# Performance work log

Hardware: AMD Instinct MI355X
Metric: run time of the kernel (lower is better)

Reference implementation:

```python
import jax, jax.numpy as jnp
import numpy as np

D_MODEL = 2048
NUM_HEADS = 16
MAX_SEQ_LEN = 2048
ROPE_BASE = 10000.0


def _rope(x, start_pos):
    # x: [B, S, D]; rotates interleaved pairs then concatenates halves,
    # exactly matching the torch module (NOT the usual interleaved output).
    B, S, D = x.shape
    theta = 1.0 / (ROPE_BASE ** (jnp.arange(0, D, 2, dtype=jnp.float32) / D))  # [D/2]
    pos = jnp.arange(start_pos, start_pos + S, dtype=jnp.float32)[:, None]      # [S,1]
    ang = pos * theta[None, :]                                                  # [S, D/2]
    cos, sin = jnp.cos(ang), jnp.sin(ang)
    x1 = x[..., 0::2]
    x2 = x[..., 1::2]
    return jnp.concatenate([x1 * cos - x2 * sin, x1 * sin + x2 * cos], axis=-1)


def setup_inputs() -> dict:
    key = jax.random.key(0)
    kx, kq, kk, kv, ko = jax.random.split(key, 5)
    B, S, D = 4, 2048, D_MODEL
    scale = 1.0 / np.sqrt(D)
    return {
        "x": jax.random.normal(kx, (B, S, D), dtype=jnp.float32),
        "w_q": jax.random.normal(kq, (D, D), dtype=jnp.float32) * scale,
        "w_k": jax.random.normal(kk, (D, D), dtype=jnp.float32) * scale,
        "w_v": jax.random.normal(kv, (D, D), dtype=jnp.float32) * scale,
        "w_o": jax.random.normal(ko, (D, D), dtype=jnp.float32) * scale,
        "start_pos": 0,
    }


def reference(x, w_q, w_k, w_v, w_o, start_pos):
    B, S, D = x.shape
    H = NUM_HEADS
    hd = D // H
    # Linear(d, d, bias=False): y = x @ W^T
    Q = _rope(x @ w_q.T, start_pos)
    K = _rope(x @ w_k.T, start_pos)
    V = x @ w_v.T
    q = Q.reshape(B, S, H, hd).transpose(0, 2, 1, 3)  # [B,H,S,hd]
    k = K.reshape(B, S, H, hd).transpose(0, 2, 1, 3)
    v = V.reshape(B, S, H, hd).transpose(0, 2, 1, 3)
    # cache=None path: kv_len == S
    attn = jnp.einsum("bhqd,bhkd->bhqk", q, k) / jnp.sqrt(jnp.float32(hd))
    # causal mask: key j attends only if j <= i + (kv_len - seq_len); here offset=0
    kv_len = k.shape[2]
    offset = kv_len - S
    i = jnp.arange(S)[:, None]
    j = jnp.arange(kv_len)[None, :]
    attn = jnp.where(j > i + offset, jnp.float32(-jnp.inf), attn)
    attn = jax.nn.softmax(attn, axis=-1)
    # dropout: inference mode (identity)
    out = jnp.einsum("bhqk,bhkd->bhqd", attn, v)
    out = out.transpose(0, 2, 1, 3).reshape(B, S, D)
    output = out @ w_o.T
    return (output, k, v)
```

## Files before the change

### kernel.cpp

```cpp
#include <hip/hip_runtime.h>
#include <hip/hip_bf16.h>

typedef __attribute__((ext_vector_type(4))) float f32x4;
typedef __attribute__((ext_vector_type(8))) short s16x8;

#define SEQ 2048
#define DM  2048
#define NH  16
#define HD  128

__device__ __forceinline__ unsigned short f2b(float f){
  unsigned int u = __builtin_bit_cast(unsigned int, f);
  u += 0x7fffu + ((u >> 16) & 1u);
  return (unsigned short)(u >> 16);
}
__device__ __forceinline__ float b2f(unsigned short h){
  unsigned int u = ((unsigned int)h) << 16;
  return __builtin_bit_cast(float, u);
}
__device__ __forceinline__ f32x4 mfma16(s16x8 a, s16x8 b, f32x4 c){
  return __builtin_amdgcn_mfma_f32_16x16x32_bf16(a, b, c, 0, 0, 0);
}

__global__ __launch_bounds__(256)
void convert_kernel(const float* __restrict__ x,  const float* __restrict__ wq,
                    const float* __restrict__ wk, const float* __restrict__ wv,
                    const float* __restrict__ wo,
                    unsigned short* __restrict__ xb,
                    unsigned short* __restrict__ wfused,
                    unsigned short* __restrict__ wob)
{
  size_t e = ((size_t)blockIdx.x * 256 + threadIdx.x) * 8;
  const float* src; unsigned short* dst;
  if (e < 16777216){ src = x + e; dst = xb + e; }
  else if (e < 29360128){
    size_t o = e - 16777216;
    int sel = (int)(o >> 22);
    const float* w = sel == 0 ? wq : (sel == 1 ? wk : wv);
    src = w + (o & 4194303); dst = wfused + o;
  } else {
    size_t o = e - 29360128;
    src = wo + o; dst = wob + o;
  }
  float4 a = ((const float4*)src)[0];
  float4 b = ((const float4*)src)[1];
  s16x8 v;
  v[0]=(short)f2b(a.x); v[1]=(short)f2b(a.y); v[2]=(short)f2b(a.z); v[3]=(short)f2b(a.w);
  v[4]=(short)f2b(b.x); v[5]=(short)f2b(b.y); v[6]=(short)f2b(b.z); v[7]=(short)f2b(b.w);
  *(s16x8*)dst = v;
}

template<int MODE>
__global__ __launch_bounds__(512, 2)
void gemm8(const unsigned short* __restrict__ A,
           const unsigned short* __restrict__ B,
           unsigned short* __restrict__ qr, unsigned short* __restrict__ kr,
           float* __restrict__ koutf,
           float* __restrict__ voutf, unsigned short* __restrict__ vt,
           float* __restrict__ outf, const int* __restrict__ sp)
{
  extern __shared__ char lds[];
  const int tid  = threadIdx.x;
  const int lane = tid & 63;
  const int w    = tid >> 6;
  const int wr   = w >> 2;
  const int wc   = w & 3;
  const int l15  = lane & 15;
  const int lhi  = lane >> 4;
  const int rq   = lhi << 2;

  int bid = blockIdx.x;
  int x8 = bid & 7, j = bid >> 3;
  int mb, nb;
  if (MODE == 0){ nb = 3*x8 + (j % 3); mb = j / 3; }
  else          { nb = x8;             mb = j; }
  const int m0 = mb * 256, n0 = nb * 256;

  const int sp0 = (MODE == 0) ? sp[0] : 0;

  const unsigned short* Abase = A + (size_t)m0 * 2048;
  const unsigned short* Bbase = B + (size_t)n0 * 2048;

  f32x4 accL[4][4] = {};
  f32x4 accH[4][4] = {};
  s16x8 af[4], bf[4];

  auto STAGE = [&](const unsigned short* gbase, int ldsoff, int t, int ks){
    #pragma unroll
    for (int r2 = 0; r2 < 2; r2++){
      int p  = r2*8192 + w*1024 + (lane << 4);
      int lo = p ^ (((p >> 7) & 3) << 4);
      int row = lo >> 6, colB = lo & 63;
      __builtin_amdgcn_global_load_lds(
        (const __attribute__((address_space(1))) void*)
          (gbase + (size_t)row*2048 + t*64 + ks*32 + (colB >> 1)),
        (__attribute__((address_space(3))) void*)(lds + ldsoff + r2*8192 + w*1024),
        16, 0, 0);
    }
  };
  auto SA = [&](int t, int ks){ STAGE(Abase, (t&1)*65536 +         ks*16384, t, ks); };
  auto SB = [&](int t, int ks){ STAGE(Bbase, (t&1)*65536 + 32768 + ks*16384, t, ks); };

  auto LDA4 = [&](int slot, int ks, int i0){
    const char* base = lds + slot*65536 + ks*16384;
    #pragma unroll
    for (int i = 0; i < 4; i++){
      int row = wr*128 + (i0 + i)*16 + l15;
      int off = row*64 + lhi*16;
      af[i] = *(const s16x8*)(base + (off ^ (((row >> 1) & 3) << 4)));
    }
  };
  auto LDB4 = [&](int slot, int ks){
    const char* base = lds + slot*65536 + 32768 + ks*16384;
    #pragma unroll
    for (int j2 = 0; j2 < 4; j2++){
      int row = wc*64 + j2*16 + l15;
      int off = row*64 + lhi*16;
      bf[j2] = *(const s16x8*)(base + (off ^ (((row >> 1) & 3) << 4)));
    }
  };
  auto MM = [&](f32x4 (&ac)[4][4]){
    __builtin_amdgcn_s_setprio(1);
    #pragma unroll
    for (int i = 0; i < 4; i++)
      #pragma unroll
      for (int j2 = 0; j2 < 4; j2++)
        ac[i][j2] = mfma16(af[i], bf[j2], ac[i][j2]);
    __builtin_amdgcn_s_setprio(0);
  };

  SA(0,0); SB(0,0); SA(0,1); SB(0,1);
  asm volatile("s_waitcnt vmcnt(4)" ::: "memory");
  __builtin_amdgcn_s_barrier();

  #pragma unroll 2
  for (int t = 0; t < 31; t++){
    const int cs = t & 1;
    LDB4(cs, 0); LDA4(cs, 0, 0);
    SA(t+1, 0);
    __builtin_amdgcn_s_barrier();
    MM(accL);
    __builtin_amdgcn_s_barrier();
    LDA4(cs, 0, 4);
    SB(t+1, 0);
    __builtin_amdgcn_s_barrier();
    MM(accH);
    asm volatile("s_waitcnt vmcnt(4)" ::: "memory");
    __builtin_amdgcn_s_barrier();
    LDB4(cs, 1); LDA4(cs, 1, 0);
    SA(t+1, 1);
    __builtin_amdgcn_s_barrier();
    MM(accL);
    __builtin_amdgcn_s_barrier();
    LDA4(cs, 1, 4);
    SB(t+1, 1);
    __builtin_amdgcn_s_barrier();
    MM(accH);
    asm volatile("s_waitcnt vmcnt(4)" ::: "memory");
    __builtin_amdgcn_s_barrier();
  }
  {
    LDB4(1, 0); LDA4(1, 0, 0);
    __builtin_amdgcn_s_barrier();
    MM(accL);
    __builtin_amdgcn_s_barrier();
    LDA4(1, 0, 4);
    __builtin_amdgcn_s_barrier();
    MM(accH);
    asm volatile("s_waitcnt vmcnt(0)" ::: "memory");
    __builtin_amdgcn_s_barrier();
    LDB4(1, 1); LDA4(1, 1, 0);
    __builtin_amdgcn_s_barrier();
    MM(accL);
    __builtin_amdgcn_s_barrier();
    LDA4(1, 1, 4);
    __builtin_amdgcn_s_barrier();
    MM(accH);
  }

  if (MODE == 1){
    #pragma unroll
    for (int h2 = 0; h2 < 2; h2++){
      f32x4 (&ac)[4][4] = h2 ? accH : accL;
      int ibase = h2 * 4;
      #pragma unroll
      for (int i = 0; i < 4; i++)
        #pragma unroll
        for (int r = 0; r < 4; r++){
          int m = m0 + wr*128 + (ibase+i)*16 + rq + r;
          #pragma unroll
          for (int j2 = 0; j2 < 4; j2++)
            outf[(size_t)m*DM + n0 + wc*64 + j2*16 + l15] = ac[i][j2][r];
        }
    }
    return;
  }

  const int b  = m0 >> 11;
  const int s0 = m0 & 2047;

  if (nb < 16){
    const bool isK = (nb >= 8);
    unsigned short* dqk = isK ? kr : qr;
    const int fbase = (nb & 7) * 128;
    const int odd = lane & 1;

    __syncthreads();
    float2* T2 = (float2*)lds;
    float2* T1 = (float2*)(lds + 32768);
    for (int idx = tid; idx < 5120; idx += 512){
      int fl = idx & 127;
      float th = exp2f(-(float)(fbase + fl) * (13.287712379549449f / 1024.0f));
      float sn, cn;
      if (idx < 4096){
        __sincosf((float)(idx >> 7) * th, &sn, &cn);
        T2[idx] = make_float2(cn, sn);
      } else {
        int sh = (idx - 4096) >> 7;
        __sincosf((float)(sp0 + s0 + sh*32) * th, &sn, &cn);
        T1[idx - 4096] = make_float2(cn, sn);
      }
    }
    __syncthreads();

    #pragma unroll
    for (int h2 = 0; h2 < 2; h2++){
      f32x4 (&ac)[4][4] = h2 ? accH : accL;
      int ibase = h2 * 4;
      #pragma unroll
      for (int i = 0; i < 4; i++){
        #pragma unroll
        for (int r = 0; r < 4; r++){
          int srow = wr*128 + (ibase+i)*16 + rq + r;
          int s  = s0 + srow;
          int sh = srow >> 5, sl = srow & 31;
          #pragma unroll
          for (int j2 = 0; j2 < 4; j2++){
            float v  = ac[i][j2][r];
            float vx = __shfl_xor(v, 1);
            int nn_loc = wc*64 + j2*16 + l15;
            int fl = nn_loc >> 1;
            float2 a1 = T1[sh*128 + fl];
            float2 a2 = T2[sl*128 + fl];
            float cn = a1.x*a2.x - a1.y*a2.y;
            float sn = a1.y*a2.x + a1.x*a2.y;
            float x1 = odd ? vx : v;
            float x2 = odd ? v  : vx;
            float ov = odd ? (x1*sn + x2*cn) : (x1*cn - x2*sn);
            int c = fbase + fl + (odd ? 1024 : 0);
            size_t adr = ((size_t)(b*NH + (c >> 7))*SEQ + s)*HD + (c & 127);
            dqk[adr] = f2b(ov);
            if (isK) koutf[adr] = ov;
          }
        }
      }
    }
  } else {
    #pragma unroll
    for (int h2 = 0; h2 < 2; h2++){
      f32x4 (&ac)[4][4] = h2 ? accH : accL;
      int ibase = h2 * 4;
      #pragma unroll
      for (int i = 0; i < 4; i++){
        int sb = s0 + wr*128 + (ibase+i)*16 + rq;
        #pragma unroll
        for (int j2 = 0; j2 < 4; j2++){
          int d = (nb - 16)*256 + wc*64 + j2*16 + l15;
          int h = d >> 7, dd = d & 127;
          size_t vb = ((size_t)(b*NH + h)*SEQ + sb)*HD + dd;
          #pragma unroll
          for (int r = 0; r < 4; r++)
            voutf[vb + (size_t)r*HD] = ac[i][j2][r];
          ushort4 pk;
          pk.x = f2b(ac[i][j2][0]); pk.y = f2b(ac[i][j2][1]);
          pk.z = f2b(ac[i][j2][2]); pk.w = f2b(ac[i][j2][3]);
          *(ushort4*)(vt + ((size_t)(b*NH + h)*HD + dd)*SEQ + sb) = pk;
        }
      }
    }
  }
}

__global__ __launch_bounds__(256)
void attn_kernel(const unsigned short* __restrict__ qr,
                 const unsigned short* __restrict__ kr,
                 const unsigned short* __restrict__ vt,
                 unsigned short* __restrict__ attnout)
{
  const int pair = blockIdx.x;
  const int bh   = blockIdx.y;
  const int tid  = threadIdx.x;
  const int lane = tid & 63;
  const int w    = tid >> 6;

  __shared__ __align__(16) char Klds[64 * 256];
  __shared__ __align__(16) char Vlds[128 * 144];
  __shared__ __align__(16) char Plds[4][16 * 144];

  const int l15 = lane & 15;
  const int lhi = lane >> 4;
  const int rq  = lhi << 2;
  char* pw = &Plds[w][0];

  s16x8 ones;
  #pragma unroll
  for (int i = 0; i < 8; i++) ones[i] = (short)0x3F80;

  const int b = bh >> 4, h = bh & 15;

  for (int ph = 0; ph < 2; ph++){
    const int qtile = ph ? (31 - pair) : pair;
    const int q0w = qtile*64 + w*16;

    s16x8 qf[4];
    const unsigned short* qbase = qr + ((size_t)bh*SEQ + q0w + l15) * HD + lhi*8;
    #pragma unroll
    for (int c = 0; c < 4; c++) qf[c] = *(const s16x8*)(qbase + c*32);

    f32x4 o[8] = {};
    f32x4 osum = {};
    float mrow[4] = {-1e30f,-1e30f,-1e30f,-1e30f};

    const int ntiles = qtile + 1;
    for (int t = 0; t < ntiles; t++){
      const int kv0 = t * 64;
      __syncthreads();
      {
        int r = tid >> 2, q4 = tid & 3;
        const unsigned short* src = kr + ((size_t)bh*SEQ + kv0 + r) * HD + q4*32;
        int sw = (r & 15) << 4;
        char* drow = Klds + r*256;
        #pragma unroll
        for (int k = 0; k < 4; k++)
          *(s16x8*)(drow + ((q4*64 + k*16) ^ sw)) = *(const s16x8*)(src + k*8);
      }
      {
        int r = tid >> 1, h2 = tid & 1;
        const unsigned short* src = vt + ((size_t)bh*HD + r) * SEQ + kv0 + h2*32;
        char* drow = Vlds + r*144 + h2*64;
        #pragma unroll
        for (int k = 0; k < 4; k++)
          *(s16x8*)(drow + k*16) = *(const s16x8*)(src + k*8);
      }
      __syncthreads();

      f32x4 st[4];
      #pragma unroll
      for (int j = 0; j < 4; j++) st[j] = (f32x4){0.f,0.f,0.f,0.f};
      #pragma unroll
      for (int j = 0; j < 4; j++){
        int krw = j*16 + l15;
        int sw  = (krw & 15) << 4;
        #pragma unroll
        for (int c = 0; c < 4; c++){
          s16x8 kf = *(const s16x8*)(Klds + krw*256 + ((c*64 + lhi*16) ^ sw));
          st[j] = mfma16(qf[c], kf, st[j]);
        }
      }

      const float sc = 0.08838834764831845f;
      #pragma unroll
      for (int j = 0; j < 4; j++)
        #pragma unroll
        for (int r = 0; r < 4; r++){
          int qrow = q0w + rq + r;
          int kvc  = kv0 + j*16 + l15;
          st[j][r] = (kvc > qrow) ? -1e30f : st[j][r] * sc;
        }

      float mt[4];
      #pragma unroll
      for (int r = 0; r < 4; r++)
        mt[r] = fmaxf(fmaxf(st[0][r], st[1][r]), fmaxf(st[2][r], st[3][r]));
      #pragma unroll
      for (int mk = 1; mk < 16; mk <<= 1)
        #pragma unroll
        for (int r = 0; r < 4; r++) mt[r] = fmaxf(mt[r], __shfl_xor(mt[r], mk));

      int ok = 1;
      #pragma unroll
      for (int r = 0; r < 4; r++) ok &= (mt[r] <= mrow[r] + 8.0f) ? 1 : 0;
      if (!__all(ok)){
        float al[4];
        #pragma unroll
        for (int r = 0; r < 4; r++){
          float mn = fmaxf(mrow[r], mt[r]);
          al[r] = __expf(mrow[r] - mn);
          mrow[r] = mn;
        }
        #pragma unroll
        for (int c = 0; c < 8; c++)
          #pragma unroll
          for (int r = 0; r < 4; r++) o[c][r] *= al[r];
        #pragma unroll
        for (int r = 0; r < 4; r++) osum[r] *= al[r];
      }

      #pragma unroll
      for (int r = 0; r < 4; r++){
        char* prb = pw + (rq + r)*144;
        #pragma unroll
        for (int j = 0; j < 4; j++){
          float p = __expf(st[j][r] - mrow[r]);
          *(unsigned short*)(prb + (j*16 + l15)*2) = f2b(p);
        }
      }

      asm volatile("s_waitcnt lgkmcnt(0)" ::: "memory");

      #pragma unroll
      for (int ks = 0; ks < 2; ks++){
        s16x8 pa = *(const s16x8*)(pw + l15*144 + ks*64 + lhi*16);
        #pragma unroll
        for (int c = 0; c < 8; c++){
          int d = c*16 + l15;
          s16x8 vf = *(const s16x8*)(Vlds + d*144 + ks*64 + lhi*16);
          o[c] = mfma16(pa, vf, o[c]);
        }
        osum = mfma16(pa, ones, osum);
      }
    }

    #pragma unroll
    for (int r = 0; r < 4; r++){
      float inv = 1.0f / osum[r];
      int s2 = q0w + rq + r;
      size_t base = ((size_t)(b*SEQ + s2)) * DM + h*HD;
      #pragma unroll
      for (int c = 0; c < 8; c++)
        attnout[base + c*16 + l15] = f2b(o[c][r] * inv);
    }
  }
}

extern "C" void kernel_launch(void* const* d_in, const int* in_sizes, int n_in,
                              void* d_out, int out_size, void* d_ws, size_t ws_size,
                              hipStream_t stream)
{
  const float* x  = (const float*)d_in[0];
  const float* wq = (const float*)d_in[1];
  const float* wk = (const float*)d_in[2];
  const float* wv = (const float*)d_in[3];
  const float* wo = (const float*)d_in[4];
  const int*   sp = (const int*)d_in[5];

  float* out  = (float*)d_out;
  float* kout = out + 16777216;
  float* vout = out + 33554432;

  char* ws = (char*)d_ws;
  unsigned short* xb      = (unsigned short*)ws;
  unsigned short* wfused  = (unsigned short*)(ws + 33554432);
  unsigned short* wob     = (unsigned short*)(ws + 58720256);
  unsigned short* qr      = (unsigned short*)(ws + 67108864);
  unsigned short* kr      = (unsigned short*)(ws + 100663296);
  unsigned short* vt      = (unsigned short*)(ws + 134217728);
  unsigned short* attnout = (unsigned short*)ws;

  hipFuncSetAttribute((const void*)gemm8<0>,
                      hipFuncAttributeMaxDynamicSharedMemorySize, 131072);
  hipFuncSetAttribute((const void*)gemm8<1>,
                      hipFuncAttributeMaxDynamicSharedMemorySize, 131072);

  convert_kernel<<<16384, 256, 0, stream>>>(x, wq, wk, wv, wo, xb, wfused, wob);
  gemm8<0><<<768, 512, 131072, stream>>>(xb, wfused, qr, kr, kout,
                                         vout, vt, nullptr, sp);
  attn_kernel<<<dim3(16, 64), 256, 0, stream>>>(qr, kr, vt, attnout);
  gemm8<1><<<256, 512, 131072, stream>>>(attnout, wob, nullptr, nullptr,
                                         nullptr, nullptr, nullptr, out, nullptr);
}
```

Baseline: 599.9 us.

## Restructure GEMM main loop into 4-stage LDS ring with one barrier per tile

```diff
diff --git a/kernel.cpp b/kernel.cpp
--- a/kernel.cpp
+++ b/kernel.cpp
@@ -51,7 +51,7 @@
 }
 
 template<int MODE>
-__global__ __launch_bounds__(512, 2)
+__global__ __launch_bounds__(512, 1)
 void gemm8(const unsigned short* __restrict__ A,
            const unsigned short* __restrict__ B,
            unsigned short* __restrict__ qr, unsigned short* __restrict__ kr,
@@ -83,9 +83,8 @@
 
   f32x4 accL[4][4] = {};
   f32x4 accH[4][4] = {};
-  s16x8 af[4], bf[4];
-
-  auto STAGE = [&](const unsigned short* gbase, int ldsoff, int t, int ks){
+
+  auto STAGE = [&](const unsigned short* gbase, int slotoff, int t){
     #pragma unroll
     for (int r2 = 0; r2 < 2; r2++){
       int p  = r2*8192 + w*1024 + (lane << 4);
@@ -93,90 +92,67 @@
       int row = lo >> 6, colB = lo & 63;
       __builtin_amdgcn_global_load_lds(
         (const __attribute__((address_space(1))) void*)
-          (gbase + (size_t)row*2048 + t*64 + ks*32 + (colB >> 1)),
-        (__attribute__((address_space(3))) void*)(lds + ldsoff + r2*8192 + w*1024),
+          (gbase + (size_t)row*2048 + t*32 + (colB >> 1)),
+        (__attribute__((address_space(3))) void*)(lds + slotoff + r2*8192 + w*1024),
         16, 0, 0);
     }
   };
-  auto SA = [&](int t, int ks){ STAGE(Abase, (t&1)*65536 +         ks*16384, t, ks); };
-  auto SB = [&](int t, int ks){ STAGE(Bbase, (t&1)*65536 + 32768 + ks*16384, t, ks); };
-
-  auto LDA4 = [&](int slot, int ks, int i0){
-    const char* base = lds + slot*65536 + ks*16384;
+  auto LDA = [&](const char* base, int i0, s16x8* dst){
     #pragma unroll
     for (int i = 0; i < 4; i++){
       int row = wr*128 + (i0 + i)*16 + l15;
       int off = row*64 + lhi*16;
-      af[i] = *(const s16x8*)(base + (off ^ (((row >> 1) & 3) << 4)));
+      dst[i] = *(const s16x8*)(base + (off ^ (((row >> 1) & 3) << 4)));
     }
   };
-  auto LDB4 = [&](int slot, int ks){
-    const char* base = lds + slot*65536 + 32768 + ks*16384;
+  auto LDB = [&](const char* base, s16x8* dst){
     #pragma unroll
     for (int j2 = 0; j2 < 4; j2++){
       int row = wc*64 + j2*16 + l15;
       int off = row*64 + lhi*16;
-      bf[j2] = *(const s16x8*)(base + (off ^ (((row >> 1) & 3) << 4)));
+      dst[j2] = *(const s16x8*)(base + (off ^ (((row >> 1) & 3) << 4)));
     }
   };
-  auto MM = [&](f32x4 (&ac)[4][4]){
+  auto MM = [&](s16x8* a, s16x8* b, f32x4 (&ac)[4][4]){
     __builtin_amdgcn_s_setprio(1);
     #pragma unroll
     for (int i = 0; i < 4; i++)
       #pragma unroll
       for (int j2 = 0; j2 < 4; j2++)
-        ac[i][j2] = mfma16(af[i], bf[j2], ac[i][j2]);
+        ac[i][j2] = mfma16(a[i], b[j2], ac[i][j2]);
     __builtin_amdgcn_s_setprio(0);
   };
 
-  SA(0,0); SB(0,0); SA(0,1); SB(0,1);
-  asm volatile("s_waitcnt vmcnt(4)" ::: "memory");
+#define TILE(T, ISSUE, VMW) { \
+    const int s_ = (T) & 3; \
+    const char* base_ = lds + s_*32768; \
+    if (ISSUE){ \
+      int so_ = (((T)+3) & 3)*32768; \
+      STAGE(Abase, so_, (T)+3); \
+      STAGE(Bbase, so_+16384, (T)+3); \
+    } \
+    s16x8 bfr[4], afL[4], afH[4]; \
+    LDB(base_+16384, bfr); LDA(base_, 0, afL); LDA(base_, 4, afH); \
+    MM(afL, bfr, accL); MM(afH, bfr, accH); \
+    asm volatile("s_waitcnt vmcnt(" #VMW ")" ::: "memory"); \
+    __builtin_amdgcn_s_barrier(); }
+
+  STAGE(Abase, 0, 0);      STAGE(Bbase, 16384, 0);
+  STAGE(Abase, 32768, 1);  STAGE(Bbase, 49152, 1);
+  STAGE(Abase, 65536, 2);  STAGE(Bbase, 81920, 2);
+  asm volatile("s_waitcnt vmcnt(8)" ::: "memory");
   __builtin_amdgcn_s_barrier();
 
-  #pragma unroll 2
-  for (int t = 0; t < 31; t++){
-    const int cs = t & 1;
-    LDB4(cs, 0); LDA4(cs, 0, 0);
-    SA(t+1, 0);
-    __builtin_amdgcn_s_barrier();
-    MM(accL);
-    __builtin_amdgcn_s_barrier();
-    LDA4(cs, 0, 4);
-    SB(t+1, 0);
-    __builtin_amdgcn_s_barrier();
-    MM(accH);
-    asm volatile("s_waitcnt vmcnt(4)" ::: "memory");
-    __builtin_amdgcn_s_barrier();
-    LDB4(cs, 1); LDA4(cs, 1, 0);
-    SA(t+1, 1);
-    __builtin_amdgcn_s_barrier();
-    MM(accL);
-    __builtin_amdgcn_s_barrier();
-    LDA4(cs, 1, 4);
-    SB(t+1, 1);
-    __builtin_amdgcn_s_barrier();
-    MM(accH);
-    asm volatile("s_waitcnt vmcnt(4)" ::: "memory");
-    __builtin_amdgcn_s_barrier();
+  for (int t = 0; t < 61; t++) TILE(t, 1, 8);
+  TILE(61, 0, 4);
+  TILE(62, 0, 0);
+  {
+    const char* base_ = lds + 3*32768;
+    s16x8 bfr[4], afL[4], afH[4];
+    LDB(base_+16384, bfr); LDA(base_, 0, afL); LDA(base_, 4, afH);
+    MM(afL, bfr, accL); MM(afH, bfr, accH);
   }
-  {
-    LDB4(1, 0); LDA4(1, 0, 0);
-    __builtin_amdgcn_s_barrier();
-    MM(accL);
-    __builtin_amdgcn_s_barrier();
-    LDA4(1, 0, 4);
-    __builtin_amdgcn_s_barrier();
-    MM(accH);
-    asm volatile("s_waitcnt vmcnt(0)" ::: "memory");
-    __builtin_amdgcn_s_barrier();
-    LDB4(1, 1); LDA4(1, 1, 0);
-    __builtin_amdgcn_s_barrier();
-    MM(accL);
-    __builtin_amdgcn_s_barrier();
-    LDA4(1, 1, 4);
-    __builtin_amdgcn_s_barrier();
-    MM(accH);
-  }
+#undef TILE
 
   if (MODE == 1){
     #pragma unroll
```

Measured after the change: 521.3 us. 13.1% less time.
